# Kernel tuning notes

Hardware: AMD Instinct MI355X
Metric: run time of the kernel (lower is better)

## Reference

```python
import jax, jax.numpy as jnp
import numpy as np

B = 4096          # events
L = 524288        # total set points (avg 128 per event)
CIN = 16          # per-point feature size (set feature 'a')
DVEC = 32         # flat feature size (feature 'b')
PHI = [128, 128, 64]
MLP = [256, 128]
EPS = 1e-5        # BatchNorm1d eps


def setup_inputs() -> dict:
    key = jax.random.key(0)
    ks = jax.random.split(key, 10)
    def n(k, shape, scale=0.05):
        return jax.random.normal(k, shape, dtype=jnp.float32) * scale
    return {
        "x_a": jax.random.normal(ks[0], (1, CIN, L), dtype=jnp.float32),
        "x_b": jax.random.normal(ks[1], (B, DVEC), dtype=jnp.float32),
        # row 0 -> counts for set feature 'a'; row 1 ignored (Reshape branch)
        "sample_indices": jnp.full((2, B), L // B, dtype=jnp.int32),
        "W1": n(ks[2], (PHI[0], CIN)),  "b1": jnp.zeros((PHI[0],), jnp.float32),
        "W2": n(ks[3], (PHI[1], PHI[0])), "b2": jnp.zeros((PHI[1],), jnp.float32),
        "W3": n(ks[4], (PHI[2], PHI[1])), "b3": jnp.zeros((PHI[2],), jnp.float32),
        "Wm1": n(ks[5], (MLP[0], PHI[2] + DVEC)), "bm1": jnp.zeros((MLP[0],), jnp.float32),
        "g1": jnp.ones((MLP[0],), jnp.float32), "be1": jnp.zeros((MLP[0],), jnp.float32),
        "Wm2": n(ks[6], (MLP[1], MLP[0])), "bm2": jnp.zeros((MLP[1],), jnp.float32),
        "g2": jnp.ones((MLP[1],), jnp.float32), "be2": jnp.zeros((MLP[1],), jnp.float32),
        "Wm3": n(ks[7], (1, MLP[1])), "bm3": jnp.zeros((1,), jnp.float32),
    }


def _bn(x, g, b):
    # BatchNorm1d, training-mode batch stats, biased variance (torch semantics)
    mu = jnp.mean(x, axis=0)
    var = jnp.var(x, axis=0)
    return (x - mu) * jax.lax.rsqrt(var + EPS) * g + b


def reference(x_a, x_b, sample_indices,
              W1, b1, W2, b2, W3, b3,
              Wm1, bm1, g1, be1, Wm2, bm2, g2, be2, Wm3, bm3):
    counts = sample_indices[0].astype(jnp.int32)                       # [B]
    bounds = jnp.concatenate([jnp.zeros((1,), jnp.int32), jnp.cumsum(counts)])  # [B+1]

    # PhiNet: pointwise Conv1d stack (kernel size 1) on [CIN, L]
    h = x_a[0]
    h = jax.nn.relu(jnp.einsum('oc,cl->ol', W1, h) + b1[:, None])
    h = jax.nn.relu(jnp.einsum('oc,cl->ol', W2, h) + b2[:, None])
    h = jax.nn.relu(jnp.einsum('oc,cl->ol', W3, h) + b3[:, None])      # [64, L]

    # fused segment-mean: point p belongs to segment j iff bounds[j] <= p < bounds[j+1]
    seg = jnp.searchsorted(bounds, jnp.arange(h.shape[1], dtype=jnp.int32), side='right') - 1
    sums = jax.ops.segment_sum(h.T, seg, num_segments=counts.shape[0])  # [B, 64]
    means = sums / jnp.maximum(counts, 1).astype(jnp.float32)[:, None]

    # feature order: sorted keys -> ('a' set repr, 'b' flat)
    z = jnp.concatenate([means, x_b.reshape(-1, DVEC)], axis=1)        # [B, 96]

    z = jax.nn.relu(_bn(z @ Wm1.T + bm1, g1, be1))
    z = jax.nn.relu(_bn(z @ Wm2.T + bm2, g2, be2))
    return jax.nn.sigmoid(z @ Wm3.T + bm3)                             # [B, 1]
```

## Files before the change

kernel.cpp:

```cpp
#include <hip/hip_runtime.h>
#include <hip/hip_bf16.h>

#define B_EVENTS 4096
#define L_PTS    524288
#define CIN      16
#define C1       128
#define C2       128
#define C3       64
#define DVEC     32
#define ZDIM     96
#define M1       256
#define M2       128
#define BN_EPS   1e-5f
#define TPTS     64
#define EPB      4

#define XOFF   0
#define H1OFF  4096
#define H2OFF  20480
#define PART   36864
#define BIAS1  37376
#define BIAS2  37888
#define BIAS3  38400
#define SCR    38656
#define SBND   38672
#define LDSSZ  38720

typedef __attribute__((ext_vector_type(8))) short bf16x8;
typedef __attribute__((ext_vector_type(4))) float f32x4;

__device__ __forceinline__ unsigned cvtpk(float lo, float hi) {
    unsigned r;
    asm("v_cvt_pk_bf16_f32 %0, %1, %2" : "=v"(r) : "v"(lo), "v"(hi));
    return r;
}

__device__ __forceinline__ unsigned long long pack4relub(f32x4 a, f32x4 b) {
    union { unsigned u[2]; unsigned long long ll; } pk;
    pk.u[0] = cvtpk(fmaxf(a[0] + b[0], 0.f), fmaxf(a[1] + b[1], 0.f));
    pk.u[1] = cvtpk(fmaxf(a[2] + b[2], 0.f), fmaxf(a[3] + b[3], 0.f));
    return pk.ll;
}

__device__ __forceinline__ bf16x8 frag_from_f32(const float* p) {
    const float4 lo = *(const float4*)p;
    const float4 hi = *(const float4*)(p + 4);
    union { unsigned u[4]; bf16x8 v; } r;
    r.u[0] = cvtpk(lo.x, lo.y);
    r.u[1] = cvtpk(lo.z, lo.w);
    r.u[2] = cvtpk(hi.x, hi.y);
    r.u[3] = cvtpk(hi.z, hi.w);
    return r.v;
}

__device__ __forceinline__ int ldsoff(int base, int rowSlots, int c, int sir) {
    int s = c * rowSlots + sir;
    s ^= (c & 7);
    return base + s * 16;
}

__global__ __launch_bounds__(256, 2) void phi_mfma_kernel(
    const float* __restrict__ xa, const float* __restrict__ xb,
    const int* __restrict__ si,
    const float* __restrict__ W1, const float* __restrict__ W2, const float* __restrict__ W3,
    const float* __restrict__ b1, const float* __restrict__ b2, const float* __restrict__ b3,
    float* __restrict__ stats, float* __restrict__ z)
{
    __shared__ __align__(16) char lds[LDSSZ];

    const int tid  = threadIdx.x;
    const int lane = tid & 63;
    const int wid  = tid >> 6;
    const int wm   = wid >> 1;
    const int wn   = wid & 1;
    const int g4   = lane >> 4;
    const int c16  = lane & 15;

    if (blockIdx.x == 0)
        for (int i = tid; i < 768; i += 256) stats[i] = 0.f;

    if (tid < 128) {
        ((float*)(lds + BIAS1))[tid] = b1[tid];
        ((float*)(lds + BIAS2))[tid] = b2[tid];
    } else if (tid < 192) {
        ((float*)(lds + BIAS3))[tid - 128] = b3[tid - 128];
    }

    const int j0 = blockIdx.x * EPB;
    {
        int psum = 0;
        for (int i = tid; i < j0; i += 256) psum += si[i];
        #pragma unroll
        for (int m = 1; m < 64; m <<= 1) psum += __shfl_xor(psum, m, 64);
        if (lane == 0) ((int*)(lds + SCR))[wid] = psum;
    }
    __syncthreads();
    if (tid == 0) {
        const int* scr = (const int*)(lds + SCR);
        int b = scr[0] + scr[1] + scr[2] + scr[3];
        int* sb = (int*)(lds + SBND);
        sb[0] = b;
        #pragma unroll
        for (int e = 0; e < EPB; ++e) { b += si[j0 + e]; sb[e + 1] = b; }
    }

    bf16x8 a1[4], a2[4][4], a3[2][4];
    {
        const bf16x8 zz = {0, 0, 0, 0, 0, 0, 0, 0};
        const int r1 = wm * 64 + c16;
        #pragma unroll
        for (int mf = 0; mf < 4; ++mf)
            a1[mf] = (g4 < 2) ? frag_from_f32(&W1[(r1 + mf * 16) * CIN + g4 * 8]) : zz;
        #pragma unroll
        for (int mf = 0; mf < 4; ++mf)
            #pragma unroll
            for (int kf = 0; kf < 4; ++kf)
                a2[mf][kf] = frag_from_f32(&W2[(r1 + mf * 16) * C1 + kf * 32 + g4 * 8]);
        const int r3 = wm * 32 + c16;
        #pragma unroll
        for (int mf = 0; mf < 2; ++mf)
            #pragma unroll
            for (int kf = 0; kf < 4; ++kf)
                a3[mf][kf] = frag_from_f32(&W3[(r3 + mf * 16) * C2 + kf * 32 + g4 * 8]);
    }
    __syncthreads();
    const int* sb = (const int*)(lds + SBND);

    const int pt = tid & 63;
    const int q  = tid >> 6;
    const int xw = pt * 32 + q * 8;

    bool staged = false;

    for (int e = 0; e < EPB; ++e) {
        const int j     = j0 + e;
        const int start = sb[e];
        const int end   = sb[e + 1];
        const int cnt   = end - start;
        const int cnt2  = (e + 1 < EPB) ? sb[e + 2] - end : 0;

        if (!staged) {
            union { unsigned u[2]; unsigned long long ll; } pk;
            const float v0 = (pt < cnt) ? xa[(size_t)(q * 4 + 0) * L_PTS + start + pt] : 0.f;
            const float v1 = (pt < cnt) ? xa[(size_t)(q * 4 + 1) * L_PTS + start + pt] : 0.f;
            const float v2 = (pt < cnt) ? xa[(size_t)(q * 4 + 2) * L_PTS + start + pt] : 0.f;
            const float v3 = (pt < cnt) ? xa[(size_t)(q * 4 + 3) * L_PTS + start + pt] : 0.f;
            pk.u[0] = cvtpk(v0, v1);
            pk.u[1] = cvtpk(v2, v3);
            *(unsigned long long*)(lds + xw) = pk.ll;
            __syncthreads();
        }

        float s[2][4];
        #pragma unroll
        for (int mf = 0; mf < 2; ++mf)
            #pragma unroll
            for (int r = 0; r < 4; ++r) s[mf][r] = 0.f;

        for (int p0 = 0; p0 < cnt; p0 += TPTS) {
            const bool inEvt  = (p0 + TPTS) < cnt;
            const bool nxtEvt = !inEvt && (e + 1 < EPB);
            const bool pre    = inEvt || nxtEvt;

            float xr0 = 0.f, xr1 = 0.f, xr2 = 0.f, xr3 = 0.f;
            if (pre) {
                const int nbase = inEvt ? (start + p0 + TPTS) : end;
                const int nrem  = inEvt ? (cnt - p0 - TPTS) : cnt2;
                xr0 = (pt < nrem) ? xa[(size_t)(q * 4 + 0) * L_PTS + nbase + pt] : 0.f;
                xr1 = (pt < nrem) ? xa[(size_t)(q * 4 + 1) * L_PTS + nbase + pt] : 0.f;
                xr2 = (pt < nrem) ? xa[(size_t)(q * 4 + 2) * L_PTS + nbase + pt] : 0.f;
                xr3 = (pt < nrem) ? xa[(size_t)(q * 4 + 3) * L_PTS + nbase + pt] : 0.f;
            }

            {
                f32x4 acc[4][2];
                #pragma unroll
                for (int mf = 0; mf < 4; ++mf) {
                    acc[mf][0] = f32x4{0.f, 0.f, 0.f, 0.f};
                    acc[mf][1] = f32x4{0.f, 0.f, 0.f, 0.f};
                }
                bf16x8 bfrag[2];
                #pragma unroll
                for (int nf = 0; nf < 2; ++nf)
                    bfrag[nf] = *(const bf16x8*)(lds + (wn * 32 + nf * 16 + c16) * 32 + g4 * 16);
                __builtin_amdgcn_s_setprio(1);
                #pragma unroll
                for (int nf = 0; nf < 2; ++nf)
                    #pragma unroll
                    for (int mf = 0; mf < 4; ++mf)
                        acc[mf][nf] = __builtin_amdgcn_mfma_f32_16x16x32_bf16(a1[mf], bfrag[nf], acc[mf][nf], 0, 0, 0);
                __builtin_amdgcn_s_setprio(0);
                #pragma unroll
                for (int mf = 0; mf < 4; ++mf) {
                    const f32x4 bb = *(const f32x4*)(lds + BIAS1 + (wm * 64 + mf * 16 + g4 * 4) * 4);
                    #pragma unroll
                    for (int nf = 0; nf < 2; ++nf) {
                        const int c = wn * 32 + nf * 16 + c16;
                        const int sir = (wm * 64 + mf * 16) / 8 + (g4 >> 1);
                        *(unsigned long long*)(lds + ldsoff(H1OFF, 16, c, sir) + (g4 & 1) * 8) = pack4relub(acc[mf][nf], bb);
                    }
                }
            }
            __syncthreads();

            {
                f32x4 acc[4][2];
                #pragma unroll
                for (int mf = 0; mf < 4; ++mf) {
                    acc[mf][0] = f32x4{0.f, 0.f, 0.f, 0.f};
                    acc[mf][1] = f32x4{0.f, 0.f, 0.f, 0.f};
                }
                #pragma unroll
                for (int nf = 0; nf < 2; ++nf) {
                    const int c = wn * 32 + nf * 16 + c16;
                    bf16x8 bk[4];
                    #pragma unroll
                    for (int kf = 0; kf < 4; ++kf)
                        bk[kf] = *(const bf16x8*)(lds + ldsoff(H1OFF, 16, c, kf * 4 + g4));
                    __builtin_amdgcn_s_setprio(1);
                    #pragma unroll
                    for (int mf = 0; mf < 4; ++mf)
                        #pragma unroll
                        for (int kf = 0; kf < 4; ++kf)
                            acc[mf][nf] = __builtin_amdgcn_mfma_f32_16x16x32_bf16(a2[mf][kf], bk[kf], acc[mf][nf], 0, 0, 0);
                    __builtin_amdgcn_s_setprio(0);
                }
                if (pre) {
                    union { unsigned u[2]; unsigned long long ll; } pk;
                    pk.u[0] = cvtpk(xr0, xr1);
                    pk.u[1] = cvtpk(xr2, xr3);
                    *(unsigned long long*)(lds + xw) = pk.ll;
                }
                #pragma unroll
                for (int mf = 0; mf < 4; ++mf) {
                    const f32x4 bb = *(const f32x4*)(lds + BIAS2 + (wm * 64 + mf * 16 + g4 * 4) * 4);
                    #pragma unroll
                    for (int nf = 0; nf < 2; ++nf) {
                        const int c = wn * 32 + nf * 16 + c16;
                        const int sir = (wm * 64 + mf * 16) / 8 + (g4 >> 1);
                        *(unsigned long long*)(lds + ldsoff(H2OFF, 16, c, sir) + (g4 & 1) * 8) = pack4relub(acc[mf][nf], bb);
                    }
                }
            }
            __syncthreads();

            {
                f32x4 acc3[2][2];
                #pragma unroll
                for (int mf = 0; mf < 2; ++mf) {
                    acc3[mf][0] = f32x4{0.f, 0.f, 0.f, 0.f};
                    acc3[mf][1] = f32x4{0.f, 0.f, 0.f, 0.f};
                }
                #pragma unroll
                for (int nf = 0; nf < 2; ++nf) {
                    const int c = wn * 32 + nf * 16 + c16;
                    bf16x8 bk[4];
                    #pragma unroll
                    for (int kf = 0; kf < 4; ++kf)
                        bk[kf] = *(const bf16x8*)(lds + ldsoff(H2OFF, 16, c, kf * 4 + g4));
                    __builtin_amdgcn_s_setprio(1);
                    #pragma unroll
                    for (int mf = 0; mf < 2; ++mf)
                        #pragma unroll
                        for (int kf = 0; kf < 4; ++kf)
                            acc3[mf][nf] = __builtin_amdgcn_mfma_f32_16x16x32_bf16(a3[mf][kf], bk[kf], acc3[mf][nf], 0, 0, 0);
                    __builtin_amdgcn_s_setprio(0);
                }
                #pragma unroll
                for (int mf = 0; mf < 2; ++mf) {
                    const f32x4 bb = *(const f32x4*)(lds + BIAS3 + (wm * 32 + mf * 16 + g4 * 4) * 4);
                    #pragma unroll
                    for (int nf = 0; nf < 2; ++nf) {
                        const int col = p0 + wn * 32 + nf * 16 + c16;
                        const bool valid = col < cnt;
                        #pragma unroll
                        for (int r = 0; r < 4; ++r) {
                            const float v = fmaxf(acc3[mf][nf][r] + bb[r], 0.f);
                            if (valid) s[mf][r] += v;
                        }
                    }
                }
            }
        }

        #pragma unroll
        for (int mf = 0; mf < 2; ++mf)
            #pragma unroll
            for (int r = 0; r < 4; ++r) {
                float v = s[mf][r];
                v += __shfl_xor(v, 1, 64);
                v += __shfl_xor(v, 2, 64);
                v += __shfl_xor(v, 4, 64);
                v += __shfl_xor(v, 8, 64);
                if (c16 == 0)
                    *(float*)(lds + PART + (wn * 64 + wm * 32 + mf * 16 + g4 * 4 + r) * 4) = v;
            }
        __syncthreads();
        {
            const float inv = 1.f / (float)max(cnt, 1);
            if (tid < C3) {
                const float v = *(const float*)(lds + PART + tid * 4)
                              + *(const float*)(lds + PART + 256 + tid * 4);
                z[(size_t)j * ZDIM + tid] = v * inv;
            } else if (tid < ZDIM) {
                z[(size_t)j * ZDIM + tid] = xb[(size_t)j * DVEC + (tid - C3)];
            }
        }

        staged = (cnt > 0) && (e + 1 < EPB);
    }
}

__global__ __launch_bounds__(256) void mlp1_kernel(
    const float* __restrict__ z, const float* __restrict__ Wm1, const float* __restrict__ bm1,
    float* __restrict__ y1, float* __restrict__ gsum, float* __restrict__ gsq)
{
    __shared__ float zs[8][ZDIM + 4];
    const int r0 = blockIdx.x * 8;
    const int tid = threadIdx.x;
    for (int i = tid; i < 8 * ZDIM; i += 256) {
        const int r = i / ZDIM, c = i - r * ZDIM;
        zs[r][c] = z[(size_t)(r0 + r) * ZDIM + c];
    }
    __syncthreads();
    const int o = tid;
    float acc[8];
    const float bb = bm1[o];
    #pragma unroll
    for (int r = 0; r < 8; ++r) acc[r] = bb;
    for (int c = 0; c < ZDIM; c += 4) {
        const float4 w = *(const float4*)&Wm1[o * ZDIM + c];
        #pragma unroll
        for (int r = 0; r < 8; ++r) {
            const float4 v = *(const float4*)&zs[r][c];
            acc[r] += w.x*v.x + w.y*v.y + w.z*v.z + w.w*v.w;
        }
    }
    float s = 0.f, sq = 0.f;
    #pragma unroll
    for (int r = 0; r < 8; ++r) {
        y1[(size_t)(r0 + r) * M1 + o] = acc[r];
        s += acc[r]; sq += acc[r] * acc[r];
    }
    atomicAdd(&gsum[o], s);
    atomicAdd(&gsq[o], sq);
}

__global__ __launch_bounds__(256) void mlp2_kernel(
    const float* __restrict__ y1,
    const float* __restrict__ gsum1, const float* __restrict__ gsq1,
    const float* __restrict__ g1, const float* __restrict__ be1,
    const float* __restrict__ Wm2, const float* __restrict__ bm2,
    float* __restrict__ y2, float* __restrict__ gsum, float* __restrict__ gsq)
{
    __shared__ float zs[8][M1 + 4];
    __shared__ float sc[M1], sh[M1];
    const int r0 = blockIdx.x * 8;
    const int tid = threadIdx.x;
    {
        const float mu  = gsum1[tid] * (1.f / B_EVENTS);
        const float var = gsq1[tid] * (1.f / B_EVENTS) - mu * mu;
        const float s0  = rsqrtf(var + BN_EPS) * g1[tid];
        sc[tid] = s0;
        sh[tid] = be1[tid] - mu * s0;
    }
    __syncthreads();
    for (int i = tid; i < 8 * M1; i += 256) {
        const int r = i >> 8, c = i & (M1 - 1);
        const float v = y1[(size_t)(r0 + r) * M1 + c];
        zs[r][c] = fmaxf(v * sc[c] + sh[c], 0.f);
    }
    __syncthreads();
    const int o = tid & 127;
    const int h = tid >> 7;
    float acc[4];
    const float bb = bm2[o];
    #pragma unroll
    for (int r = 0; r < 4; ++r) acc[r] = bb;
    for (int c = 0; c < M1; c += 4) {
        const float4 w = *(const float4*)&Wm2[o * M1 + c];
        #pragma unroll
        for (int r = 0; r < 4; ++r) {
            const float4 v = *(const float4*)&zs[h * 4 + r][c];
            acc[r] += w.x*v.x + w.y*v.y + w.z*v.z + w.w*v.w;
        }
    }
    float s = 0.f, sq = 0.f;
    #pragma unroll
    for (int r = 0; r < 4; ++r) {
        y2[(size_t)(r0 + h * 4 + r) * M2 + o] = acc[r];
        s += acc[r]; sq += acc[r] * acc[r];
    }
    atomicAdd(&gsum[o], s);
    atomicAdd(&gsq[o], sq);
}

__global__ __launch_bounds__(256) void final_kernel(
    const float* __restrict__ y2,
    const float* __restrict__ gsum2, const float* __restrict__ gsq2,
    const float* __restrict__ g2, const float* __restrict__ be2,
    const float* __restrict__ Wm3, const float* __restrict__ bm3,
    float* __restrict__ out)
{
    __shared__ float sc[M2], sh[M2];
    const int tid = threadIdx.x;
    if (tid < M2) {
        const float mu  = gsum2[tid] * (1.f / B_EVENTS);
        const float var = gsq2[tid] * (1.f / B_EVENTS) - mu * mu;
        const float s0  = rsqrtf(var + BN_EPS) * g2[tid];
        sc[tid] = s0;
        sh[tid] = be2[tid] - mu * s0;
    }
    __syncthreads();
    const int w = tid >> 6, l = tid & 63;
    const int r = blockIdx.x * 4 + w;
    const float e0 = fmaxf(y2[(size_t)r * M2 + l]      * sc[l]      + sh[l],      0.f);
    const float e1 = fmaxf(y2[(size_t)r * M2 + 64 + l] * sc[64 + l] + sh[64 + l], 0.f);
    float a = e0 * Wm3[l] + e1 * Wm3[64 + l];
    #pragma unroll
    for (int off = 32; off >= 1; off >>= 1) a += __shfl_down(a, off, 64);
    if (l == 0) out[r] = 1.f / (1.f + expf(-(a + bm3[0])));
}

extern "C" void kernel_launch(void* const* d_in, const int* in_sizes, int n_in,
                              void* d_out, int out_size, void* d_ws, size_t ws_size,
                              hipStream_t stream) {
    const float* xa  = (const float*)d_in[0];
    const float* xb  = (const float*)d_in[1];
    const int*   si  = (const int*)  d_in[2];
    const float* W1  = (const float*)d_in[3];
    const float* b1  = (const float*)d_in[4];
    const float* W2  = (const float*)d_in[5];
    const float* b2  = (const float*)d_in[6];
    const float* W3  = (const float*)d_in[7];
    const float* b3  = (const float*)d_in[8];
    const float* Wm1 = (const float*)d_in[9];
    const float* bm1 = (const float*)d_in[10];
    const float* g1  = (const float*)d_in[11];
    const float* be1 = (const float*)d_in[12];
    const float* Wm2 = (const float*)d_in[13];
    const float* bm2 = (const float*)d_in[14];
    const float* g2  = (const float*)d_in[15];
    const float* be2 = (const float*)d_in[16];
    const float* Wm3 = (const float*)d_in[17];
    const float* bm3 = (const float*)d_in[18];
    float* out = (float*)d_out;

    char* ws = (char*)d_ws;
    size_t off = 0;
    auto alloc = [&](size_t bytes) -> void* {
        void* p = ws + off;
        off = (off + bytes + 255) & ~(size_t)255;
        return p;
    };
    float* stats = (float*)alloc(768 * sizeof(float));
    float* z     = (float*)alloc((size_t)B_EVENTS * ZDIM * sizeof(float));
    float* y1    = (float*)alloc((size_t)B_EVENTS * M1 * sizeof(float));
    float* y2    = (float*)alloc((size_t)B_EVENTS * M2 * sizeof(float));
    float* gsum1 = stats;
    float* gsq1  = stats + 256;
    float* gsum2 = stats + 512;
    float* gsq2  = stats + 640;

    hipLaunchKernelGGL(phi_mfma_kernel, dim3(B_EVENTS / EPB), dim3(256), 0, stream,
                       xa, xb, si, W1, W2, W3, b1, b2, b3, stats, z);
    hipLaunchKernelGGL(mlp1_kernel, dim3(B_EVENTS / 8), dim3(256), 0, stream,
                       z, Wm1, bm1, y1, gsum1, gsq1);
    hipLaunchKernelGGL(mlp2_kernel, dim3(B_EVENTS / 8), dim3(256), 0, stream,
                       y1, gsum1, gsq1, g1, be1, Wm2, bm2, y2, gsum2, gsq2);
    hipLaunchKernelGGL(final_kernel, dim3(B_EVENTS / 4), dim3(256), 0, stream,
                       y2, gsum2, gsq2, g2, be2, Wm3, bm3, out);
}
```

Baseline: 142.3 us.

## Split phi work into fixed point tiles with atomic segment sums

Replaces the per-block event loop (4 events per block, serial 64-point tiles, prefix sum recomputed in every block) with a separate single-block scan that builds event bounds and a tile-to-event map. The phi kernel then runs one 64-point tile per block, with each wave owning an output-row slice, and accumulates per-event sums into a global buffer using atomics. A fast path reduces in-wave when a tile lies inside one event. The mean division and the xb concatenation move into the first MLP kernel. This gives more, evenly sized blocks and drops the serial per-event loop, at the cost of an extra launch, a memset and atomic traffic, and it also loses the prefetch overlap of the next tile.

```diff
diff --git a/kernel.cpp b/kernel.cpp
--- a/kernel.cpp
+++ b/kernel.cpp
@@ -12,19 +12,14 @@
 #define M1       256
 #define M2       128
 #define BN_EPS   1e-5f
-#define TPTS     64
-#define EPB      4
-
-#define XOFF   0
-#define H1OFF  4096
-#define H2OFF  20480
-#define PART   36864
-#define BIAS1  37376
-#define BIAS2  37888
-#define BIAS3  38400
-#define SCR    38656
-#define SBND   38672
-#define LDSSZ  38720
+#define TILE     64
+#define NTILES   (L_PTS / TILE)
+
+#define XSTRIDE  72
+#define XOFF     0
+#define H1OFF    4608
+#define H2OFF    20992
+#define LDSSZ    37376
 
 typedef __attribute__((ext_vector_type(8))) short bf16x8;
 typedef __attribute__((ext_vector_type(4))) float f32x4;
@@ -59,260 +54,230 @@
     return base + s * 16;
 }
 
-__global__ __launch_bounds__(256, 2) void phi_mfma_kernel(
-    const float* __restrict__ xa, const float* __restrict__ xb,
-    const int* __restrict__ si,
+__global__ __launch_bounds__(1024) void scan_kernel(const int* __restrict__ si,
+                                                    int* __restrict__ bounds,
+                                                    int* __restrict__ tilemap)
+{
+    __shared__ int sh[1024];
+    const int tid = threadIdx.x;
+    const int c0 = si[tid*4+0], c1 = si[tid*4+1], c2 = si[tid*4+2], c3 = si[tid*4+3];
+    const int s4 = c0 + c1 + c2 + c3;
+    sh[tid] = s4;
+    __syncthreads();
+    for (int off = 1; off < 1024; off <<= 1) {
+        int add = (tid >= off) ? sh[tid - off] : 0;
+        __syncthreads();
+        sh[tid] += add;
+        __syncthreads();
+    }
+    const int excl = (tid == 0) ? 0 : sh[tid - 1];
+    bounds[tid*4+0] = excl;
+    bounds[tid*4+1] = excl + c0;
+    bounds[tid*4+2] = excl + c0 + c1;
+    bounds[tid*4+3] = excl + c0 + c1 + c2;
+    if (tid == 1023) bounds[B_EVENTS] = excl + s4;
+    __syncthreads();
+
+    const int total = bounds[B_EVENTS];
+    for (int t = tid; t < NTILES; t += 1024) {
+        const int p0 = t * TILE;
+        if (p0 >= total) { tilemap[t] = -1; continue; }
+        int e = (int)(((long long)p0 * B_EVENTS) / total);
+        if (e > B_EVENTS - 1) e = B_EVENTS - 1;
+        while (bounds[e] > p0) --e;
+        while (bounds[e + 1] <= p0) ++e;
+        const bool fast = (p0 + TILE <= bounds[e + 1]);
+        tilemap[t] = e | (fast ? (1 << 30) : 0);
+    }
+}
+
+__global__ __launch_bounds__(256, 3) void phi_mfma_kernel(
+    const float* __restrict__ xa,
+    const int* __restrict__ bounds, const int* __restrict__ tilemap,
     const float* __restrict__ W1, const float* __restrict__ W2, const float* __restrict__ W3,
     const float* __restrict__ b1, const float* __restrict__ b2, const float* __restrict__ b3,
-    float* __restrict__ stats, float* __restrict__ z)
+    float* __restrict__ zsum)
 {
     __shared__ __align__(16) char lds[LDSSZ];
 
     const int tid  = threadIdx.x;
     const int lane = tid & 63;
-    const int wid  = tid >> 6;
-    const int wm   = wid >> 1;
-    const int wn   = wid & 1;
+    const int wm   = tid >> 6;
     const int g4   = lane >> 4;
     const int c16  = lane & 15;
 
-    if (blockIdx.x == 0)
-        for (int i = tid; i < 768; i += 256) stats[i] = 0.f;
-
-    if (tid < 128) {
-        ((float*)(lds + BIAS1))[tid] = b1[tid];
-        ((float*)(lds + BIAS2))[tid] = b2[tid];
-    } else if (tid < 192) {
-        ((float*)(lds + BIAS3))[tid - 128] = b3[tid - 128];
-    }
-
-    const int j0 = blockIdx.x * EPB;
-    {
-        int psum = 0;
-        for (int i = tid; i < j0; i += 256) psum += si[i];
-        #pragma unroll
-        for (int m = 1; m < 64; m <<= 1) psum += __shfl_xor(psum, m, 64);
-        if (lane == 0) ((int*)(lds + SCR))[wid] = psum;
-    }
-    __syncthreads();
-    if (tid == 0) {
-        const int* scr = (const int*)(lds + SCR);
-        int b = scr[0] + scr[1] + scr[2] + scr[3];
-        int* sb = (int*)(lds + SBND);
-        sb[0] = b;
-        #pragma unroll
-        for (int e = 0; e < EPB; ++e) { b += si[j0 + e]; sb[e + 1] = b; }
-    }
-
-    bf16x8 a1[4], a2[4][4], a3[2][4];
+    const int tm = tilemap[blockIdx.x];
+    if (tm < 0) return;
+    const int  e0    = tm & 0x3FFFFFFF;
+    const bool fastp = (tm >> 30) & 1;
+    const int  p0    = blockIdx.x * TILE;
+
+    const int pt = tid & 63;
+    const int h  = tid >> 6;
+    float xv[4];
+    #pragma unroll
+    for (int jj = 0; jj < 4; ++jj)
+        xv[jj] = xa[(size_t)(h * 4 + jj) * L_PTS + p0 + pt];
+
+    f32x4 bb1[2], bb2[2], bb3;
+    #pragma unroll
+    for (int mf = 0; mf < 2; ++mf) {
+        bb1[mf] = *(const f32x4*)&b1[wm * 32 + mf * 16 + g4 * 4];
+        bb2[mf] = *(const f32x4*)&b2[wm * 32 + mf * 16 + g4 * 4];
+    }
+    bb3 = *(const f32x4*)&b3[wm * 16 + g4 * 4];
+
+    bf16x8 a1[2], a2[2][4], a3[4];
     {
         const bf16x8 zz = {0, 0, 0, 0, 0, 0, 0, 0};
-        const int r1 = wm * 64 + c16;
-        #pragma unroll
-        for (int mf = 0; mf < 4; ++mf)
+        const int r1 = wm * 32 + c16;
+        #pragma unroll
+        for (int mf = 0; mf < 2; ++mf)
             a1[mf] = (g4 < 2) ? frag_from_f32(&W1[(r1 + mf * 16) * CIN + g4 * 8]) : zz;
         #pragma unroll
-        for (int mf = 0; mf < 4; ++mf)
+        for (int mf = 0; mf < 2; ++mf)
             #pragma unroll
             for (int kf = 0; kf < 4; ++kf)
                 a2[mf][kf] = frag_from_f32(&W2[(r1 + mf * 16) * C1 + kf * 32 + g4 * 8]);
-        const int r3 = wm * 32 + c16;
+        const int r3 = wm * 16 + c16;
+        #pragma unroll
+        for (int kf = 0; kf < 4; ++kf)
+            a3[kf] = frag_from_f32(&W3[r3 * C2 + kf * 32 + g4 * 8]);
+    }
+
+    {
+        union { unsigned u[2]; unsigned long long ll; } pk;
+        pk.u[0] = cvtpk(xv[0], xv[1]);
+        pk.u[1] = cvtpk(xv[2], xv[3]);
+        *(unsigned long long*)(lds + XOFF + pt * XSTRIDE + h * 8) = pk.ll;
+        *(unsigned long long*)(lds + XOFF + (tid >> 2) * XSTRIDE + 32 + (tid & 3) * 8) = 0ull;
+    }
+    __syncthreads();
+
+    {
+        f32x4 acc[2][4];
         #pragma unroll
         for (int mf = 0; mf < 2; ++mf)
             #pragma unroll
+            for (int nf = 0; nf < 4; ++nf)
+                acc[mf][nf] = f32x4{0.f, 0.f, 0.f, 0.f};
+        bf16x8 bfr[4];
+        #pragma unroll
+        for (int nf = 0; nf < 4; ++nf)
+            bfr[nf] = *(const bf16x8*)(lds + XOFF + (nf * 16 + c16) * XSTRIDE + g4 * 16);
+        __builtin_amdgcn_s_setprio(1);
+        #pragma unroll
+        for (int nf = 0; nf < 4; ++nf)
+            #pragma unroll
+            for (int mf = 0; mf < 2; ++mf)
+                acc[mf][nf] = __builtin_amdgcn_mfma_f32_16x16x32_bf16(a1[mf], bfr[nf], acc[mf][nf], 0, 0, 0);
+        __builtin_amdgcn_s_setprio(0);
+        #pragma unroll
+        for (int mf = 0; mf < 2; ++mf) {
+            const int sir = wm * 4 + mf * 2 + (g4 >> 1);
+            #pragma unroll
+            for (int nf = 0; nf < 4; ++nf) {
+                const int c = nf * 16 + c16;
+                *(unsigned long long*)(lds + ldsoff(H1OFF, 16, c, sir) + (g4 & 1) * 8) = pack4relub(acc[mf][nf], bb1[mf]);
+            }
+        }
+    }
+    __syncthreads();
+
+    {
+        f32x4 acc[2][4];
+        #pragma unroll
+        for (int mf = 0; mf < 2; ++mf)
+            #pragma unroll
+            for (int nf = 0; nf < 4; ++nf)
+                acc[mf][nf] = f32x4{0.f, 0.f, 0.f, 0.f};
+        #pragma unroll
+        for (int nf = 0; nf < 4; ++nf) {
+            const int c = nf * 16 + c16;
+            bf16x8 bk[4];
+            #pragma unroll
             for (int kf = 0; kf < 4; ++kf)
-                a3[mf][kf] = frag_from_f32(&W3[(r3 + mf * 16) * C2 + kf * 32 + g4 * 8]);
-    }
-    __syncthreads();
-    const int* sb = (const int*)(lds + SBND);
-
-    const int pt = tid & 63;
-    const int q  = tid >> 6;
-    const int xw = pt * 32 + q * 8;
-
-    bool staged = false;
-
-    for (int e = 0; e < EPB; ++e) {
-        const int j     = j0 + e;
-        const int start = sb[e];
-        const int end   = sb[e + 1];
-        const int cnt   = end - start;
-        const int cnt2  = (e + 1 < EPB) ? sb[e + 2] - end : 0;
-
-        if (!staged) {
-            union { unsigned u[2]; unsigned long long ll; } pk;
-            const float v0 = (pt < cnt) ? xa[(size_t)(q * 4 + 0) * L_PTS + start + pt] : 0.f;
-            const float v1 = (pt < cnt) ? xa[(size_t)(q * 4 + 1) * L_PTS + start + pt] : 0.f;
-            const float v2 = (pt < cnt) ? xa[(size_t)(q * 4 + 2) * L_PTS + start + pt] : 0.f;
-            const float v3 = (pt < cnt) ? xa[(size_t)(q * 4 + 3) * L_PTS + start + pt] : 0.f;
-            pk.u[0] = cvtpk(v0, v1);
-            pk.u[1] = cvtpk(v2, v3);
-            *(unsigned long long*)(lds + xw) = pk.ll;
-            __syncthreads();
-        }
-
-        float s[2][4];
-        #pragma unroll
-        for (int mf = 0; mf < 2; ++mf)
-            #pragma unroll
-            for (int r = 0; r < 4; ++r) s[mf][r] = 0.f;
-
-        for (int p0 = 0; p0 < cnt; p0 += TPTS) {
-            const bool inEvt  = (p0 + TPTS) < cnt;
-            const bool nxtEvt = !inEvt && (e + 1 < EPB);
-            const bool pre    = inEvt || nxtEvt;
-
-            float xr0 = 0.f, xr1 = 0.f, xr2 = 0.f, xr3 = 0.f;
-            if (pre) {
-                const int nbase = inEvt ? (start + p0 + TPTS) : end;
-                const int nrem  = inEvt ? (cnt - p0 - TPTS) : cnt2;
-                xr0 = (pt < nrem) ? xa[(size_t)(q * 4 + 0) * L_PTS + nbase + pt] : 0.f;
-                xr1 = (pt < nrem) ? xa[(size_t)(q * 4 + 1) * L_PTS + nbase + pt] : 0.f;
-                xr2 = (pt < nrem) ? xa[(size_t)(q * 4 + 2) * L_PTS + nbase + pt] : 0.f;
-                xr3 = (pt < nrem) ? xa[(size_t)(q * 4 + 3) * L_PTS + nbase + pt] : 0.f;
+                bk[kf] = *(const bf16x8*)(lds + ldsoff(H1OFF, 16, c, kf * 4 + g4));
+            __builtin_amdgcn_s_setprio(1);
+            #pragma unroll
+            for (int mf = 0; mf < 2; ++mf)
+                #pragma unroll
+                for (int kf = 0; kf < 4; ++kf)
+                    acc[mf][nf] = __builtin_amdgcn_mfma_f32_16x16x32_bf16(a2[mf][kf], bk[kf], acc[mf][nf], 0, 0, 0);
+            __builtin_amdgcn_s_setprio(0);
+        }
+        #pragma unroll
+        for (int mf = 0; mf < 2; ++mf) {
+            const int sir = wm * 4 + mf * 2 + (g4 >> 1);
+            #pragma unroll
+            for (int nf = 0; nf < 4; ++nf) {
+                const int c = nf * 16 + c16;
+                *(unsigned long long*)(lds + ldsoff(H2OFF, 16, c, sir) + (g4 & 1) * 8) = pack4relub(acc[mf][nf], bb2[mf]);
             }
-
-            {
-                f32x4 acc[4][2];
+        }
+    }
+    __syncthreads();
+
+    {
+        f32x4 acc3[4];
+        #pragma unroll
+        for (int nf = 0; nf < 4; ++nf) acc3[nf] = f32x4{0.f, 0.f, 0.f, 0.f};
+        #pragma unroll
+        for (int nf = 0; nf < 4; ++nf) {
+            const int c = nf * 16 + c16;
+            bf16x8 bk[4];
+            #pragma unroll
+            for (int kf = 0; kf < 4; ++kf)
+                bk[kf] = *(const bf16x8*)(lds + ldsoff(H2OFF, 16, c, kf * 4 + g4));
+            __builtin_amdgcn_s_setprio(1);
+            #pragma unroll
+            for (int kf = 0; kf < 4; ++kf)
+                acc3[nf] = __builtin_amdgcn_mfma_f32_16x16x32_bf16(a3[kf], bk[kf], acc3[nf], 0, 0, 0);
+            __builtin_amdgcn_s_setprio(0);
+        }
+
+        if (fastp) {
+            float s[4] = {0.f, 0.f, 0.f, 0.f};
+            #pragma unroll
+            for (int nf = 0; nf < 4; ++nf)
                 #pragma unroll
-                for (int mf = 0; mf < 4; ++mf) {
-                    acc[mf][0] = f32x4{0.f, 0.f, 0.f, 0.f};
-                    acc[mf][1] = f32x4{0.f, 0.f, 0.f, 0.f};
-                }
-                bf16x8 bfrag[2];
-                #pragma unroll
-                for (int nf = 0; nf < 2; ++nf)
-                    bfrag[nf] = *(const bf16x8*)(lds + (wn * 32 + nf * 16 + c16) * 32 + g4 * 16);
-                __builtin_amdgcn_s_setprio(1);
-                #pragma unroll
-                for (int nf = 0; nf < 2; ++nf)
-                    #pragma unroll
-                    for (int mf = 0; mf < 4; ++mf)
-                        acc[mf][nf] = __builtin_amdgcn_mfma_f32_16x16x32_bf16(a1[mf], bfrag[nf], acc[mf][nf], 0, 0, 0);
-                __builtin_amdgcn_s_setprio(0);
-                #pragma unroll
-                for (int mf = 0; mf < 4; ++mf) {
-                    const f32x4 bb = *(const f32x4*)(lds + BIAS1 + (wm * 64 + mf * 16 + g4 * 4) * 4);
-                    #pragma unroll
-                    for (int nf = 0; nf < 2; ++nf) {
-                        const int c = wn * 32 + nf * 16 + c16;
-                        const int sir = (wm * 64 + mf * 16) / 8 + (g4 >> 1);
-                        *(unsigned long long*)(lds + ldsoff(H1OFF, 16, c, sir) + (g4 & 1) * 8) = pack4relub(acc[mf][nf], bb);
-                    }
-                }
-            }
-            __syncthreads();
-
-            {
-                f32x4 acc[4][2];
-                #pragma unroll
-                for (int mf = 0; mf < 4; ++mf) {
-                    acc[mf][0] = f32x4{0.f, 0.f, 0.f, 0.f};
-                    acc[mf][1] = f32x4{0.f, 0.f, 0.f, 0.f};
-                }
-                #pragma unroll
-                for (int nf = 0; nf < 2; ++nf) {
-                    const int c = wn * 32 + nf * 16 + c16;
-                    bf16x8 bk[4];
-                    #pragma unroll
-                    for (int kf = 0; kf < 4; ++kf)
-                        bk[kf] = *(const bf16x8*)(lds + ldsoff(H1OFF, 16, c, kf * 4 + g4));
-                    __builtin_amdgcn_s_setprio(1);
-                    #pragma unroll
-                    for (int mf = 0; mf < 4; ++mf)
-                        #pragma unroll
-                        for (int kf = 0; kf < 4; ++kf)
-                            acc[mf][nf] = __builtin_amdgcn_mfma_f32_16x16x32_bf16(a2[mf][kf], bk[kf], acc[mf][nf], 0, 0, 0);
-                    __builtin_amdgcn_s_setprio(0);
-                }
-                if (pre) {
-                    union { unsigned u[2]; unsigned long long ll; } pk;
-                    pk.u[0] = cvtpk(xr0, xr1);
-                    pk.u[1] = cvtpk(xr2, xr3);
-                    *(unsigned long long*)(lds + xw) = pk.ll;
-                }
-                #pragma unroll
-                for (int mf = 0; mf < 4; ++mf) {
-                    const f32x4 bb = *(const f32x4*)(lds + BIAS2 + (wm * 64 + mf * 16 + g4 * 4) * 4);
-                    #pragma unroll
-                    for (int nf = 0; nf < 2; ++nf) {
-                        const int c = wn * 32 + nf * 16 + c16;
-                        const int sir = (wm * 64 + mf * 16) / 8 + (g4 >> 1);
-                        *(unsigned long long*)(lds + ldsoff(H2OFF, 16, c, sir) + (g4 & 1) * 8) = pack4relub(acc[mf][nf], bb);
-                    }
-                }
-            }
-            __syncthreads();
-
-            {
-                f32x4 acc3[2][2];
-                #pragma unroll
-                for (int mf = 0; mf < 2; ++mf) {
-                    acc3[mf][0] = f32x4{0.f, 0.f, 0.f, 0.f};
-                    acc3[mf][1] = f32x4{0.f, 0.f, 0.f, 0.f};
-                }
-                #pragma unroll
-                for (int nf = 0; nf < 2; ++nf) {
-                    const int c = wn * 32 + nf * 16 + c16;
-                    bf16x8 bk[4];
-                    #pragma unroll
-                    for (int kf = 0; kf < 4; ++kf)
-                        bk[kf] = *(const bf16x8*)(lds + ldsoff(H2OFF, 16, c, kf * 4 + g4));
-                    __builtin_amdgcn_s_setprio(1);
-                    #pragma unroll
-                    for (int mf = 0; mf < 2; ++mf)
-                        #pragma unroll
-                        for (int kf = 0; kf < 4; ++kf)
-                            acc3[mf][nf] = __builtin_amdgcn_mfma_f32_16x16x32_bf16(a3[mf][kf], bk[kf], acc3[mf][nf], 0, 0, 0);
-                    __builtin_amdgcn_s_setprio(0);
-                }
-                #pragma unroll
-                for (int mf = 0; mf < 2; ++mf) {
-                    const f32x4 bb = *(const f32x4*)(lds + BIAS3 + (wm * 32 + mf * 16 + g4 * 4) * 4);
-                    #pragma unroll
-                    for (int nf = 0; nf < 2; ++nf) {
-                        const int col = p0 + wn * 32 + nf * 16 + c16;
-                        const bool valid = col < cnt;
-                        #pragma unroll
-                        for (int r = 0; r < 4; ++r) {
-                            const float v = fmaxf(acc3[mf][nf][r] + bb[r], 0.f);
-                            if (valid) s[mf][r] += v;
-                        }
-                    }
-                }
-            }
-        }
-
-        #pragma unroll
-        for (int mf = 0; mf < 2; ++mf)
+                for (int r = 0; r < 4; ++r)
+                    s[r] += fmaxf(acc3[nf][r] + bb3[r], 0.f);
             #pragma unroll
             for (int r = 0; r < 4; ++r) {
-                float v = s[mf][r];
+                float v = s[r];
                 v += __shfl_xor(v, 1, 64);
                 v += __shfl_xor(v, 2, 64);
                 v += __shfl_xor(v, 4, 64);
                 v += __shfl_xor(v, 8, 64);
-                if (c16 == 0)
-                    *(float*)(lds + PART + (wn * 64 + wm * 32 + mf * 16 + g4 * 4 + r) * 4) = v;
+                s[r] = v;
             }
-        __syncthreads();
-        {
-            const float inv = 1.f / (float)max(cnt, 1);
-            if (tid < C3) {
-                const float v = *(const float*)(lds + PART + tid * 4)
-                              + *(const float*)(lds + PART + 256 + tid * 4);
-                z[(size_t)j * ZDIM + tid] = v * inv;
-            } else if (tid < ZDIM) {
-                z[(size_t)j * ZDIM + tid] = xb[(size_t)j * DVEC + (tid - C3)];
+            if (c16 == 0) {
+                #pragma unroll
+                for (int r = 0; r < 4; ++r)
+                    atomicAdd(&zsum[(size_t)e0 * C3 + wm * 16 + g4 * 4 + r], s[r]);
             }
-        }
-
-        staged = (cnt > 0) && (e + 1 < EPB);
+        } else {
+            const int total = bounds[B_EVENTS];
+            #pragma unroll
+            for (int nf = 0; nf < 4; ++nf) {
+                const int col = p0 + nf * 16 + c16;
+                if (col < total) {
+                    int sgr = e0;
+                    while (col >= bounds[sgr + 1]) ++sgr;
+                    #pragma unroll
+                    for (int r = 0; r < 4; ++r)
+                        atomicAdd(&zsum[(size_t)sgr * C3 + wm * 16 + g4 * 4 + r],
+                                  fmaxf(acc3[nf][r] + bb3[r], 0.f));
+                }
+            }
+        }
     }
 }
 
 __global__ __launch_bounds__(256) void mlp1_kernel(
-    const float* __restrict__ z, const float* __restrict__ Wm1, const float* __restrict__ bm1,
+    const float* __restrict__ zsum, const int* __restrict__ si, const float* __restrict__ xb,
+    const float* __restrict__ Wm1, const float* __restrict__ bm1,
     float* __restrict__ y1, float* __restrict__ gsum, float* __restrict__ gsq)
 {
     __shared__ float zs[8][ZDIM + 4];
@@ -320,7 +285,14 @@
     const int tid = threadIdx.x;
     for (int i = tid; i < 8 * ZDIM; i += 256) {
         const int r = i / ZDIM, c = i - r * ZDIM;
-        zs[r][c] = z[(size_t)(r0 + r) * ZDIM + c];
+        float v;
+        if (c < C3) {
+            const int cnt = si[r0 + r];
+            v = zsum[(size_t)(r0 + r) * C3 + c] / (float)max(cnt, 1);
+        } else {
+            v = xb[(size_t)(r0 + r) * DVEC + (c - C3)];
+        }
+        zs[r][c] = v;
     }
     __syncthreads();
     const int o = tid;
@@ -453,19 +425,24 @@
         off = (off + bytes + 255) & ~(size_t)255;
         return p;
     };
-    float* stats = (float*)alloc(768 * sizeof(float));
-    float* z     = (float*)alloc((size_t)B_EVENTS * ZDIM * sizeof(float));
-    float* y1    = (float*)alloc((size_t)B_EVENTS * M1 * sizeof(float));
-    float* y2    = (float*)alloc((size_t)B_EVENTS * M2 * sizeof(float));
+    float* zsum    = (float*)alloc((size_t)B_EVENTS * C3 * sizeof(float));
+    float* stats   = (float*)alloc(768 * sizeof(float));
+    int*   bounds  = (int*)  alloc((B_EVENTS + 1) * sizeof(int));
+    int*   tilemap = (int*)  alloc(NTILES * sizeof(int));
+    float* y1      = (float*)alloc((size_t)B_EVENTS * M1 * sizeof(float));
+    float* y2      = (float*)alloc((size_t)B_EVENTS * M2 * sizeof(float));
     float* gsum1 = stats;
     float* gsq1  = stats + 256;
     float* gsum2 = stats + 512;
     float* gsq2  = stats + 640;
 
-    hipLaunchKernelGGL(phi_mfma_kernel, dim3(B_EVENTS / EPB), dim3(256), 0, stream,
-                       xa, xb, si, W1, W2, W3, b1, b2, b3, stats, z);
+    hipMemsetAsync(zsum, 0, (size_t)B_EVENTS * C3 * sizeof(float) + 768 * sizeof(float), stream);
+
+    hipLaunchKernelGGL(scan_kernel, dim3(1), dim3(1024), 0, stream, si, bounds, tilemap);
+    hipLaunchKernelGGL(phi_mfma_kernel, dim3(NTILES), dim3(256), 0, stream,
+                       xa, bounds, tilemap, W1, W2, W3, b1, b2, b3, zsum);
     hipLaunchKernelGGL(mlp1_kernel, dim3(B_EVENTS / 8), dim3(256), 0, stream,
-                       z, Wm1, bm1, y1, gsum1, gsq1);
+                       zsum, si, xb, Wm1, bm1, y1, gsum1, gsq1);
     hipLaunchKernelGGL(mlp2_kernel, dim3(B_EVENTS / 8), dim3(256), 0, stream,
                        y1, gsum1, gsq1, g1, be1, Wm2, bm2, y2, gsum2, gsq2);
     hipLaunchKernelGGL(final_kernel, dim3(B_EVENTS / 4), dim3(256), 0, stream,
```

Result: slower. 185.5 us (+30.4%).
